# Kernel tuning notes

Hardware: AMD Instinct MI355X
Metric: run time of the kernel (lower is better)

## Reference

```python
import jax, jax.numpy as jnp
import numpy as np

N_NODES = 100000
N_EDGES = 800000
NUM_GRAPHS = 512
IN_DIM = 16
EDGE_DIM = 1
HID = 64       # emb_dim
MLP_H = 32     # hidden_layers inside each MPNNLayer
L = 3          # num_layers
EPS = 1e-5


def setup_inputs() -> dict:
    key = jax.random.key(0)
    ks = jax.random.split(key, 24)
    s = 0.05
    inp = {
        "x": jax.random.normal(ks[0], (N_NODES, IN_DIM), jnp.float32),
        "edge_index": jax.random.randint(ks[1], (2, N_EDGES), 0, N_NODES),
        "edge_attr": jax.random.uniform(ks[2], (N_EDGES, EDGE_DIM), jnp.float32),
        "batch": jnp.sort(jax.random.randint(ks[3], (N_NODES,), 0, NUM_GRAPHS)),
        # input projection
        "lin_in_w": jax.random.normal(ks[4], (IN_DIM, HID), jnp.float32) * s,
        "lin_in_b": jnp.zeros((HID,), jnp.float32),
        # message MLP (stacked over L layers): Linear(129->32), BN(32), ReLU, Linear(32->64), ReLU, BN(64)
        "msg_w1": jax.random.normal(ks[5], (L, 2 * HID + EDGE_DIM, MLP_H), jnp.float32) * s,
        "msg_b1": jnp.zeros((L, MLP_H), jnp.float32),
        "msg_g1": jnp.ones((L, MLP_H), jnp.float32),
        "msg_be1": jnp.zeros((L, MLP_H), jnp.float32),
        "msg_w2": jax.random.normal(ks[6], (L, MLP_H, HID), jnp.float32) * s,
        "msg_b2": jnp.zeros((L, HID), jnp.float32),
        "msg_g2": jnp.ones((L, HID), jnp.float32),
        "msg_be2": jnp.zeros((L, HID), jnp.float32),
        # update MLP: Linear(128->32), BN(32), ReLU, Linear(32->64), ReLU, BN(64)
        "upd_w1": jax.random.normal(ks[7], (L, 2 * HID, MLP_H), jnp.float32) * s,
        "upd_b1": jnp.zeros((L, MLP_H), jnp.float32),
        "upd_g1": jnp.ones((L, MLP_H), jnp.float32),
        "upd_be1": jnp.zeros((L, MLP_H), jnp.float32),
        "upd_w2": jax.random.normal(ks[8], (L, MLP_H, HID), jnp.float32) * s,
        "upd_b2": jnp.zeros((L, HID), jnp.float32),
        "upd_g2": jnp.ones((L, HID), jnp.float32),
        "upd_be2": jnp.zeros((L, HID), jnp.float32),
        # head Linear(64->1) + ReLU
        "out_w": jax.random.normal(ks[9], (HID, 1), jnp.float32) * s,
        "out_b": jnp.zeros((1,), jnp.float32),
    }
    return inp


def _bn(h, g, b):
    # BatchNorm1d, training-mode batch stats (biased variance), dropout treated as identity (eval)
    mu = jnp.mean(h, axis=0)
    var = jnp.var(h, axis=0)
    return g * (h - mu) * jax.lax.rsqrt(var + EPS) + b


def reference(x, edge_index, edge_attr, batch,
              lin_in_w, lin_in_b,
              msg_w1, msg_b1, msg_g1, msg_be1, msg_w2, msg_b2, msg_g2, msg_be2,
              upd_w1, upd_b1, upd_g1, upd_be1, upd_w2, upd_b2, upd_g2, upd_be2,
              out_w, out_b):
    src = edge_index[0]  # x_j source
    dst = edge_index[1]  # x_i target / aggregation index
    h = x @ lin_in_w + lin_in_b  # [N, HID]
    for l in range(L):
        # message: cat([x_i, x_j, edge_attr]) -> Linear -> BN -> ReLU -> Linear -> ReLU -> BN
        m_in = jnp.concatenate([h[dst], h[src], edge_attr], axis=1)  # [E, 2*HID+EDGE_DIM]
        m = jax.nn.relu(_bn(m_in @ msg_w1[l] + msg_b1[l], msg_g1[l], msg_be1[l]))
        m = _bn(jax.nn.relu(m @ msg_w2[l] + msg_b2[l]), msg_g2[l], msg_be2[l])
        # aggregate: scatter-add over destination nodes
        agg = jax.ops.segment_sum(m, dst, num_segments=N_NODES)  # [N, HID]
        # update: cat([x, aggr]) -> Linear -> BN -> ReLU -> Linear -> ReLU -> BN
        u_in = jnp.concatenate([h, agg], axis=1)  # [N, 2*HID]
        u = jax.nn.relu(_bn(u_in @ upd_w1[l] + upd_b1[l], upd_g1[l], upd_be1[l]))
        u = _bn(jax.nn.relu(u @ upd_w2[l] + upd_b2[l]), upd_g2[l], upd_be2[l])
        h = h + u  # residual (x += conv(...))
    # global mean pool
    pooled = jax.ops.segment_sum(h, batch, num_segments=NUM_GRAPHS)
    counts = jax.ops.segment_sum(jnp.ones((h.shape[0],), h.dtype), batch, num_segments=NUM_GRAPHS)
    pooled = pooled / jnp.maximum(counts, 1.0)[:, None]
    return jax.nn.relu(pooled @ out_w + out_b).reshape(-1)  # [NUM_GRAPHS]
```

## Files before the change

### kernel.cpp

```cpp
#include <hip/hip_runtime.h>
#include <hip/hip_bf16.h>

#define N_NODES   100000
#define N_EDGES   800000
#define NUM_GRAPHS 512
#define IN_DIM    16
#define HID       64
#define MLP_H     32
#define EPS       1e-5f
#define TPB       256
#define SCAN_B    1024
#define NCHUNK    ((N_NODES + SCAN_B - 1) / SCAN_B)
#define GSB       2048
#define NWAVES    (GSB * 4)
#define PER_W     ((N_EDGES + NWAVES - 1) / NWAVES)
#define NODEBLKS  ((N_NODES + 63) / 64)

using nh2   = decltype(__builtin_amdgcn_cvt_pkrtz(0.f, 0.f));
typedef _Float16 f16x8 __attribute__((ext_vector_type(8)));
typedef float    f32x4 __attribute__((ext_vector_type(4)));
typedef int      i32x4 __attribute__((ext_vector_type(4)));

__device__ __forceinline__ nh2 pack2(float a, float b) {
  return __builtin_amdgcn_cvt_pkrtz(a, b);
}
__device__ __forceinline__ float wsum(float v) {
  v += __shfl_xor(v, 1, 64);
  v += __shfl_xor(v, 2, 64);
  v += __shfl_xor(v, 4, 64);
  v += __shfl_xor(v, 8, 64);
  v += __shfl_xor(v, 16, 64);
  v += __shfl_xor(v, 32, 64);
  return v;
}
__device__ __forceinline__ int lbound(const int* __restrict__ rs, int key) {
  int lo = 0, hi = N_NODES;
  while (lo < hi) { int m = (lo + hi) >> 1; if (rs[m] < key) lo = m + 1; else hi = m; }
  return lo;
}

__global__ __launch_bounds__(TPB) void k_deg(const int* __restrict__ ei, int* __restrict__ deg) {
  int e = blockIdx.x * TPB + threadIdx.x;
  if (e < N_EDGES) atomicAdd(&deg[ei[N_EDGES + e]], 1);
}

__global__ __launch_bounds__(SCAN_B) void k_scan_part(const int* __restrict__ deg,
                                                      int* __restrict__ partials) {
  __shared__ int red[SCAN_B];
  int i = blockIdx.x * SCAN_B + threadIdx.x;
  red[threadIdx.x] = (i < N_NODES) ? deg[i] : 0;
  __syncthreads();
  for (int off = SCAN_B / 2; off > 0; off >>= 1) {
    if (threadIdx.x < off) red[threadIdx.x] += red[threadIdx.x + off];
    __syncthreads();
  }
  if (threadIdx.x == 0) partials[blockIdx.x] = red[0];
}

__global__ void k_scan_mid(int* __restrict__ partials, int* __restrict__ row_start) {
  int run = 0;
  for (int b = 0; b < NCHUNK; ++b) { int t = partials[b]; partials[b] = run; run += t; }
  row_start[N_NODES] = run;
}

__global__ __launch_bounds__(SCAN_B) void k_scan_fin(const int* __restrict__ deg,
                                                     const int* __restrict__ partials,
                                                     int* __restrict__ row_start,
                                                     int* __restrict__ cursor) {
  __shared__ int buf[2][SCAN_B];
  int t = threadIdx.x, i = blockIdx.x * SCAN_B + t;
  int v = (i < N_NODES) ? deg[i] : 0;
  buf[0][t] = v;
  __syncthreads();
  int cur = 0;
  for (int off = 1; off < SCAN_B; off <<= 1) {
    int nv = buf[cur][t] + ((t >= off) ? buf[cur][t - off] : 0);
    buf[cur ^ 1][t] = nv; cur ^= 1;
    __syncthreads();
  }
  if (i < N_NODES) {
    int excl = buf[cur][t] - v + partials[blockIdx.x];
    row_start[i] = excl;
    cursor[i] = excl;
  }
}

__global__ __launch_bounds__(TPB) void k_fill(const int* __restrict__ ei,
                                              const float* __restrict__ ea,
                                              int* __restrict__ cursor,
                                              i32x4* __restrict__ erec) {
  int e = blockIdx.x * TPB + threadIdx.x;
  if (e >= N_EDGES) return;
  int dst = ei[N_EDGES + e];
  int pos = atomicAdd(&cursor[dst], 1);
  i32x4 rec;
  rec[0] = ei[e];
  rec[1] = dst;
  rec[2] = __float_as_int(ea[e]);
  rec[3] = 0;
  erec[pos] = rec;
}

__global__ __launch_bounds__(TPB) void k_lin_in(const float* __restrict__ x,
                                                const float* __restrict__ w,
                                                const float* __restrict__ b,
                                                float* __restrict__ h) {
  int i = blockIdx.x * TPB + threadIdx.x;
  if (i >= N_NODES) return;
  float xi[IN_DIM];
  const float4* xp = reinterpret_cast<const float4*>(x + i * IN_DIM);
#pragma unroll
  for (int q = 0; q < 4; ++q) {
    float4 v = xp[q];
    xi[4*q] = v.x; xi[4*q+1] = v.y; xi[4*q+2] = v.z; xi[4*q+3] = v.w;
  }
  float4* hp = reinterpret_cast<float4*>(h + i * HID);
#pragma unroll
  for (int j4 = 0; j4 < HID/4; ++j4) {
    float o[4];
#pragma unroll
    for (int c = 0; c < 4; ++c) {
      int j = j4*4 + c;
      float acc = b[j];
#pragma unroll
      for (int k = 0; k < IN_DIM; ++k) acc += xi[k] * w[k*HID + j];
      o[c] = acc;
    }
    float4 ov = {o[0], o[1], o[2], o[3]};
    hp[j4] = ov;
  }
}

__global__ __launch_bounds__(TPB) void k_pq(const float* __restrict__ h,
                                            const float* __restrict__ w1,
                                            const float* __restrict__ b1,
                                            float* __restrict__ P,
                                            _Float16* __restrict__ Qh) {
  const int part = __builtin_amdgcn_readfirstlane(threadIdx.x >> 6);
  const int lane = threadIdx.x & 63;
  const int i = blockIdx.x * 64 + lane;
  if (i >= N_NODES) return;
  const int jb = (part & 1) * 16;
  const bool isQ = part >= 2;
  const float* wbase = w1 + (isQ ? 64 * MLP_H : 0) + jb;
  float acc[16];
#pragma unroll
  for (int j = 0; j < 16; ++j) acc[j] = isQ ? 0.f : b1[jb + j];
  const float4* hp = reinterpret_cast<const float4*>(h + i * HID);
#pragma unroll 4
  for (int k4 = 0; k4 < 16; ++k4) {
    float4 a = hp[k4];
    const float* wr = wbase + (k4*4) * MLP_H;
#pragma unroll
    for (int j = 0; j < 16; ++j)
      acc[j] += a.x*wr[j] + a.y*wr[MLP_H+j] + a.z*wr[2*MLP_H+j] + a.w*wr[3*MLP_H+j];
  }
  if (!isQ) {
    float4* pp = reinterpret_cast<float4*>(P + i * MLP_H + jb);
#pragma unroll
    for (int c = 0; c < 4; ++c) {
      float4 o = {acc[4*c], acc[4*c+1], acc[4*c+2], acc[4*c+3]};
      pp[c] = o;
    }
  } else {
    i32x4 o0, o1;
#pragma unroll
    for (int c = 0; c < 4; ++c) {
      o0[c] = __builtin_bit_cast(int, pack2(acc[2*c],     acc[2*c+1]));
      o1[c] = __builtin_bit_cast(int, pack2(acc[8+2*c],   acc[8+2*c+1]));
    }
    i32x4* qp = reinterpret_cast<i32x4*>(Qh + i * MLP_H + jb);
    qp[0] = o0; qp[1] = o1;
  }
}

__global__ __launch_bounds__(TPB) void k_gather(const float* __restrict__ P,
                                                const _Float16* __restrict__ Qh,
                                                const i32x4* __restrict__ erec,
                                                const float* __restrict__ w1,
                                                _Float16* __restrict__ z1h,
                                                float* __restrict__ gstat) {
  const int lane = threadIdx.x & 63;
  const int kq  = lane & 15;
  const int qtr = lane >> 4;
  const float wk0 = w1[128 * MLP_H + 2*kq];
  const float wk1 = w1[128 * MLP_H + 2*kq + 1];
  const int* Qi = (const int*)Qh;
  int* z1i = (int*)z1h;
  float s0 = 0.f, s1 = 0.f, qa0 = 0.f, qa1 = 0.f;
  const int wv = blockIdx.x * 4 + (threadIdx.x >> 6);
  const int c0 = wv * PER_W;
  const int c1 = min(c0 + PER_W, N_EDGES);
  if (c0 < N_EDGES) {
    const int c1m1 = c1 - 1;
    const int rounds = (c1 - c0 + 3) >> 2;
#define EIDX(R) min(c0 + 4*(R) + qtr, c1m1)
    i32x4 rec2 = erec[EIDX(0)];
    i32x4 rec3 = erec[EIDX(1)];
    i32x4 recH = erec[EIDX(2)];
    int   qiA = Qi[rec2[0] * 16 + kq];
    float2 pA = *reinterpret_cast<const float2*>(P + rec2[1] * MLP_H + 2*kq);
    float  aA = __int_as_float(rec2[2]);
    int   qiB = Qi[rec3[0] * 16 + kq];
    float2 pB = *reinterpret_cast<const float2*>(P + rec3[1] * MLP_H + 2*kq);
    float  aB = __int_as_float(rec3[2]);
    for (int r = 0; r < rounds; ++r) {
      i32x4 recN = erec[EIDX(r + 3)];
      int   qiC = Qi[recH[0] * 16 + kq];
      float2 pC = *reinterpret_cast<const float2*>(P + recH[1] * MLP_H + 2*kq);
      float  aC = __int_as_float(recH[2]);
      const int e = c0 + 4*r + qtr;
      nh2 hv = __builtin_bit_cast(nh2, qiA);
      float z0 = pA.x + (float)hv.x + aA * wk0;
      float z1 = pA.y + (float)hv.y + aA * wk1;
      if (e < c1) {
        z1i[min(e, c1m1) * 16 + kq] = __builtin_bit_cast(int, pack2(z0, z1));
        s0 += z0; s1 += z1;
        qa0 = fmaf(z0, z0, qa0); qa1 = fmaf(z1, z1, qa1);
      }
      qiA = qiB; pA = pB; aA = aB;
      qiB = qiC; pB = pC; aB = aC;
      recH = recN;
    }
#undef EIDX
  }
  s0  += __shfl_xor(s0, 16, 64);  s0  += __shfl_xor(s0, 32, 64);
  s1  += __shfl_xor(s1, 16, 64);  s1  += __shfl_xor(s1, 32, 64);
  qa0 += __shfl_xor(qa0, 16, 64); qa0 += __shfl_xor(qa0, 32, 64);
  qa1 += __shfl_xor(qa1, 16, 64); qa1 += __shfl_xor(qa1, 32, 64);
  __shared__ float ls[4][MLP_H], lq[4][MLP_H];
  const int w = threadIdx.x >> 6;
  if (lane < 16) {
    ls[w][2*lane] = s0; ls[w][2*lane+1] = s1;
    lq[w][2*lane] = qa0; lq[w][2*lane+1] = qa1;
  }
  __syncthreads();
  const int t = threadIdx.x;
  if (t < MLP_H)
    unsafeAtomicAdd(&gstat[t], ls[0][t] + ls[1][t] + ls[2][t] + ls[3][t]);
  else if (t < 2*MLP_H)
    unsafeAtomicAdd(&gstat[t], lq[0][t-MLP_H] + lq[1][t-MLP_H] + lq[2][t-MLP_H] + lq[3][t-MLP_H]);
}

__global__ __launch_bounds__(TPB) void k_msgdot(const _Float16* __restrict__ z1h,
                                                const int* __restrict__ rs,
                                                const float* __restrict__ gstat_in,
                                                const float* __restrict__ g1,
                                                const float* __restrict__ be1,
                                                const float* __restrict__ w2,
                                                const float* __restrict__ b2,
                                                float* __restrict__ agg,
                                                float* __restrict__ gstat_out) {
  const int lane = threadIdx.x & 63;
  const int col = lane & 15;
  const int g   = lane >> 4;
  float a1v[8], c1v[8];
#pragma unroll
  for (int i = 0; i < 8; ++i) {
    int kf = g*8 + i;
    float mu = gstat_in[kf] * (1.f / N_EDGES);
    float var = fmaxf(gstat_in[MLP_H + kf] * (1.f / N_EDGES) - mu * mu, 0.f);
    float a = g1[kf] * rsqrtf(var + EPS);
    a1v[i] = a; c1v[i] = be1[kf] - a * mu;
  }
  f16x8 bf0, bf1, bf2, bf3;
#define MKB(BF, C) { i32x4 bw; \
  _Pragma("unroll") for (int ii = 0; ii < 4; ++ii) { \
    nh2 p = pack2(w2[(g*8 + 2*ii) * HID + (C)*16 + col], \
                  w2[(g*8 + 2*ii + 1) * HID + (C)*16 + col]); \
    bw[ii] = __builtin_bit_cast(int, p); } \
  BF = __builtin_bit_cast(f16x8, bw); }
  MKB(bf0, 0) MKB(bf1, 1) MKB(bf2, 2) MKB(bf3, 3)
#undef MKB
  float b2c[4];
#pragma unroll
  for (int c = 0; c < 4; ++c) b2c[c] = b2[c*16 + col];

  float sacc[4] = {0.f,0.f,0.f,0.f}, qacc[4] = {0.f,0.f,0.f,0.f};
  const int wv = blockIdx.x * 4 + (threadIdx.x >> 6);
  const int key0 = min(wv * PER_W, N_EDGES);
  const int key1 = min((wv + 1) * PER_W, N_EDGES);
  const int n0 = lbound(rs, key0);
  const int n1 = (wv == NWAVES - 1) ? N_NODES : lbound(rs, key1);

  for (int n = n0; n < n1; ++n) {
    const int start = rs[n], end = rs[n + 1];
    float aggacc[4] = {0.f,0.f,0.f,0.f};
    for (int t0 = start; t0 < end; t0 += 16) {
      const int ec = min(t0 + col, end - 1);
      f16x8 zv = *reinterpret_cast<const f16x8*>(z1h + ec * MLP_H + g * 8);
      i32x4 aw;
#pragma unroll
      for (int i = 0; i < 4; ++i) {
        float m0 = fmaxf(fmaf(a1v[2*i],   (float)zv[2*i],   c1v[2*i]),   0.f);
        float m1 = fmaxf(fmaf(a1v[2*i+1], (float)zv[2*i+1], c1v[2*i+1]), 0.f);
        aw[i] = __builtin_bit_cast(int, pack2(m0, m1));
      }
      f16x8 af = __builtin_bit_cast(f16x8, aw);
      f32x4 zc = {0.f,0.f,0.f,0.f};
      f32x4 cc0 = __builtin_amdgcn_mfma_f32_16x16x32_f16(af, bf0, zc, 0, 0, 0);
      f32x4 cc1 = __builtin_amdgcn_mfma_f32_16x16x32_f16(af, bf1, zc, 0, 0, 0);
      f32x4 cc2 = __builtin_amdgcn_mfma_f32_16x16x32_f16(af, bf2, zc, 0, 0, 0);
      f32x4 cc3 = __builtin_amdgcn_mfma_f32_16x16x32_f16(af, bf3, zc, 0, 0, 0);
      bool vld[4];
#pragma unroll
      for (int reg = 0; reg < 4; ++reg) vld[reg] = (t0 + g*4 + reg) < end;
#define EPI(CC, CI) { \
  _Pragma("unroll") for (int reg = 0; reg < 4; ++reg) { \
    float tv = fmaxf(CC[reg] + b2c[CI], 0.f); \
    tv = vld[reg] ? tv : 0.f; \
    aggacc[CI] += tv; qacc[CI] = fmaf(tv, tv, qacc[CI]); } }
      EPI(cc0, 0) EPI(cc1, 1) EPI(cc2, 2) EPI(cc3, 3)
#undef EPI
    }
#pragma unroll
    for (int c = 0; c < 4; ++c) sacc[c] += aggacc[c];
#pragma unroll
    for (int c = 0; c < 4; ++c) {
      aggacc[c] += __shfl_xor(aggacc[c], 16, 64);
      aggacc[c] += __shfl_xor(aggacc[c], 32, 64);
    }
    float aout = (g == 0) ? aggacc[0] : (g == 1) ? aggacc[1] : (g == 2) ? aggacc[2] : aggacc[3];
    agg[n * HID + g * 16 + col] = aout;
  }
#pragma unroll
  for (int c = 0; c < 4; ++c) {
    sacc[c] += __shfl_xor(sacc[c], 16, 64);
    sacc[c] += __shfl_xor(sacc[c], 32, 64);
    qacc[c] += __shfl_xor(qacc[c], 16, 64);
    qacc[c] += __shfl_xor(qacc[c], 32, 64);
  }
  __shared__ float ls[4][HID], lq[4][HID];
  const int w = threadIdx.x >> 6;
  if (g == 0) {
#pragma unroll
    for (int c = 0; c < 4; ++c) { ls[w][c*16 + col] = sacc[c]; lq[w][c*16 + col] = qacc[c]; }
  }
  __syncthreads();
  const int t = threadIdx.x;
  if (t < HID)
    unsafeAtomicAdd(&gstat_out[t], ls[0][t] + ls[1][t] + ls[2][t] + ls[3][t]);
  else if (t < 2*HID)
    unsafeAtomicAdd(&gstat_out[t], lq[0][t-HID] + lq[1][t-HID] + lq[2][t-HID] + lq[3][t-HID]);
}

__global__ __launch_bounds__(TPB) void k_upd1(const float* __restrict__ h,
                                              const float* __restrict__ agg,
                                              const int* __restrict__ deg,
                                              const float* __restrict__ gstat_in,
                                              const float* __restrict__ g2,
                                              const float* __restrict__ be2,
                                              const float* __restrict__ w1,
                                              const float* __restrict__ b1,
                                              float* __restrict__ zu1) {
  __shared__ float sa[HID], sc[HID];
  {
    int t = threadIdx.x;
    if (t < HID) {
      float mu = gstat_in[t] * (1.f / N_EDGES);
      float var = fmaxf(gstat_in[HID + t] * (1.f / N_EDGES) - mu * mu, 0.f);
      float a = g2[t] * rsqrtf(var + EPS);
      sa[t] = a; sc[t] = be2[t] - a * mu;
    }
  }
  __syncthreads();
  const int widx = __builtin_amdgcn_readfirstlane(threadIdx.x >> 6);
  const int part = widx & 1;
  const int grp  = blockIdx.x * 2 + (widx >> 1);
  const int lane = threadIdx.x & 63;
  const int jb = part * 16;
  const int i = grp * 64 + lane;
  if (i >= N_NODES) return;
  float acc[16];
#pragma unroll
  for (int j = 0; j < 16; ++j) acc[j] = b1[jb + j];
  const float4* hp = reinterpret_cast<const float4*>(h + i * HID);
#pragma unroll 4
  for (int k4 = 0; k4 < 16; ++k4) {
    float4 a = hp[k4];
    const float* wr = w1 + (k4*4) * MLP_H + jb;
#pragma unroll
    for (int j = 0; j < 16; ++j)
      acc[j] += a.x*wr[j] + a.y*wr[MLP_H+j] + a.z*wr[2*MLP_H+j] + a.w*wr[3*MLP_H+j];
  }
  float degf = (float)deg[i];
  const float4* ap = reinterpret_cast<const float4*>(agg + i * HID);
#pragma unroll 4
  for (int k4 = 0; k4 < 16; ++k4) {
    float4 g4 = ap[k4];
    int k = k4*4;
    float a0 = sa[k]  *g4.x + sc[k]  *degf;
    float a1 = sa[k+1]*g4.y + sc[k+1]*degf;
    float a2 = sa[k+2]*g4.z + sc[k+2]*degf;
    float a3 = sa[k+3]*g4.w + sc[k+3]*degf;
    const float* wr = w1 + (64 + k) * MLP_H + jb;
#pragma unroll
    for (int j = 0; j < 16; ++j)
      acc[j] += a0*wr[j] + a1*wr[MLP_H+j] + a2*wr[2*MLP_H+j] + a3*wr[3*MLP_H+j];
  }
  float4* zp = reinterpret_cast<float4*>(zu1 + i * MLP_H + jb);
#pragma unroll
  for (int c = 0; c < 4; ++c) {
    float4 o = {acc[4*c], acc[4*c+1], acc[4*c+2], acc[4*c+3]};
    zp[c] = o;
  }
}

__global__ __launch_bounds__(TPB) void k_upd2(const float* __restrict__ zu1,
                                              const float* __restrict__ gstat_in,
                                              const float* __restrict__ gu1,
                                              const float* __restrict__ beu1,
                                              const float* __restrict__ w2,
                                              const float* __restrict__ b2,
                                              float* __restrict__ tu) {
  __shared__ float sa[MLP_H], sc[MLP_H];
  {
    int t = threadIdx.x;
    if (t < MLP_H) {
      float mu = gstat_in[t] * (1.f / N_NODES);
      float var = fmaxf(gstat_in[MLP_H + t] * (1.f / N_NODES) - mu * mu, 0.f);
      float a = gu1[t] * rsqrtf(var + EPS);
      sa[t] = a; sc[t] = beu1[t] - a * mu;
    }
  }
  __syncthreads();
  const int widx = __builtin_amdgcn_readfirstlane(threadIdx.x >> 6);
  const int part = widx & 1;
  const int grp  = blockIdx.x * 2 + (widx >> 1);
  const int lane = threadIdx.x & 63;
  const int jb = part * 32;
  const int i = grp * 64 + lane;
  if (i >= N_NODES) return;
  float m1[MLP_H];
  const float4* zp = reinterpret_cast<const float4*>(zu1 + i * MLP_H);
#pragma unroll
  for (int c = 0; c < MLP_H/4; ++c) {
    float4 z = zp[c];
    int kk = 4*c;
    m1[kk]   = fmaxf(sa[kk]  *z.x + sc[kk],   0.f);
    m1[kk+1] = fmaxf(sa[kk+1]*z.y + sc[kk+1], 0.f);
    m1[kk+2] = fmaxf(sa[kk+2]*z.z + sc[kk+2], 0.f);
    m1[kk+3] = fmaxf(sa[kk+3]*z.w + sc[kk+3], 0.f);
  }
#pragma unroll
  for (int j4 = 0; j4 < 8; ++j4) {
    float tv[4];
#pragma unroll
    for (int c = 0; c < 4; ++c) {
      int j = jb + j4*4 + c;
      float v = b2[j];
#pragma unroll
      for (int kk = 0; kk < MLP_H; ++kk) v += m1[kk] * w2[kk*HID + j];
      tv[c] = fmaxf(v, 0.f);
    }
    float4 o = {tv[0], tv[1], tv[2], tv[3]};
    *reinterpret_cast<float4*>(tu + i * HID + jb + j4*4) = o;
  }
}

template <int NF>
__global__ __launch_bounds__(TPB) void k_colstats(const float* __restrict__ X,
                                                  int nrows, float* __restrict__ gstat) {
  const int RPB = TPB / NF;
  int f = threadIdx.x % NF;
  int rloc = threadIdx.x / NF;
  float s = 0.f, q = 0.f;
  for (int r = blockIdx.x * RPB + rloc; r < nrows; r += gridDim.x * RPB) {
    float v = X[r * NF + f];
    s += v; q = fmaf(v, v, q);
  }
  __shared__ float ls[TPB], lq[TPB];
  ls[threadIdx.x] = s; lq[threadIdx.x] = q;
  __syncthreads();
  if (threadIdx.x < NF) {
    float ss = 0.f, qq = 0.f;
#pragma unroll
    for (int r = 0; r < RPB; ++r) { ss += ls[r*NF + f]; qq += lq[r*NF + f]; }
    unsafeAtomicAdd(&gstat[f], ss);
    unsafeAtomicAdd(&gstat[NF + f], qq);
  }
}

__global__ __launch_bounds__(TPB) void k_resid(float* __restrict__ h,
                                               const float* __restrict__ tu,
                                               const float* __restrict__ gstat_in,
                                               const float* __restrict__ gu2,
                                               const float* __restrict__ beu2) {
  __shared__ float sa[HID], sc[HID];
  {
    int t = threadIdx.x;
    if (t < HID) {
      float mu = gstat_in[t] * (1.f / N_NODES);
      float var = fmaxf(gstat_in[HID + t] * (1.f / N_NODES) - mu * mu, 0.f);
      float a = gu2[t] * rsqrtf(var + EPS);
      sa[t] = a; sc[t] = beu2[t] - a * mu;
    }
  }
  __syncthreads();
  int idx = blockIdx.x * TPB + threadIdx.x;
  if (idx >= N_NODES * (HID/4)) return;
  int j0 = (idx & (HID/4 - 1)) * 4;
  float4 hv = reinterpret_cast<const float4*>(h)[idx];
  float4 tv = reinterpret_cast<const float4*>(tu)[idx];
  hv.x += sa[j0]  *tv.x + sc[j0];
  hv.y += sa[j0+1]*tv.y + sc[j0+1];
  hv.z += sa[j0+2]*tv.z + sc[j0+2];
  hv.w += sa[j0+3]*tv.w + sc[j0+3];
  reinterpret_cast<float4*>(h)[idx] = hv;
}

__global__ __launch_bounds__(TPB) void k_pool_head(const float* __restrict__ h,
                                                   const int* __restrict__ batch,
                                                   const float* __restrict__ ow,
                                                   const float* __restrict__ ob,
                                                   float* __restrict__ out) {
  int g = blockIdx.x;
  int lo = 0, hi = N_NODES;
  while (lo < hi) { int mid = (lo+hi) >> 1; if (batch[mid] < g) lo = mid+1; else hi = mid; }
  int start = lo;
  lo = start; hi = N_NODES;
  while (lo < hi) { int mid = (lo+hi) >> 1; if (batch[mid] < g+1) lo = mid+1; else hi = mid; }
  int end = lo;
  int j = threadIdx.x & 63;
  int sub = threadIdx.x >> 6;
  float acc = 0.f;
  for (int n = start + sub; n < end; n += 4) acc += h[n*HID + j];
  __shared__ float red[TPB];
  red[threadIdx.x] = acc;
  __syncthreads();
  if (threadIdx.x < 64) {
    float s = red[threadIdx.x] + red[64+threadIdx.x] + red[128+threadIdx.x] + red[192+threadIdx.x];
    float cnt = (float)(end - start);
    float pooled = s / fmaxf(cnt, 1.0f);
    float v = pooled * ow[threadIdx.x];
    v = wsum(v);
    if (threadIdx.x == 0) out[g] = fmaxf(v + ob[0], 0.f);
  }
}

extern "C" void kernel_launch(void* const* d_in, const int* in_sizes, int n_in,
                              void* d_out, int out_size, void* d_ws, size_t ws_size,
                              hipStream_t stream) {
  const float* x       = (const float*)d_in[0];
  const int*   ei      = (const int*)  d_in[1];
  const float* ea      = (const float*)d_in[2];
  const int*   batch   = (const int*)  d_in[3];
  const float* lin_w   = (const float*)d_in[4];
  const float* lin_b   = (const float*)d_in[5];
  const float* msg_w1  = (const float*)d_in[6];
  const float* msg_b1  = (const float*)d_in[7];
  const float* msg_g1  = (const float*)d_in[8];
  const float* msg_be1 = (const float*)d_in[9];
  const float* msg_w2  = (const float*)d_in[10];
  const float* msg_b2  = (const float*)d_in[11];
  const float* msg_g2  = (const float*)d_in[12];
  const float* msg_be2 = (const float*)d_in[13];
  const float* upd_w1  = (const float*)d_in[14];
  const float* upd_b1  = (const float*)d_in[15];
  const float* upd_g1  = (const float*)d_in[16];
  const float* upd_be1 = (const float*)d_in[17];
  const float* upd_w2  = (const float*)d_in[18];
  const float* upd_b2  = (const float*)d_in[19];
  const float* upd_g2  = (const float*)d_in[20];
  const float* upd_be2 = (const float*)d_in[21];
  const float* out_w   = (const float*)d_in[22];
  const float* out_b   = (const float*)d_in[23];
  float* out = (float*)d_out;

  float* W     = (float*)d_ws;
  float* h     = W;
  float* P     = W + 6400000;
  _Float16* Qh = (_Float16*)(W + 9600000);
  float* agg   = W + 12800000;
  _Float16* z1h = (_Float16*)(W + 19200000);
  float* zu1   = W + 32000000;
  float* tu    = W + 35200000;
  float* stats = W + 41600000;
  int*   ib    = (int*)(W + 41601152);
  int* deg       = ib;
  int* row_start = ib + 100000;
  int* cursor    = ib + 200001;
  int* partials  = ib + 300001;
  i32x4* erec    = (i32x4*)(ib + 300232);

  hipMemsetAsync(stats, 0, 3*384*sizeof(float), stream);
  hipMemsetAsync(deg, 0, N_NODES*sizeof(int), stream);

  k_deg<<<N_EDGES/TPB, TPB, 0, stream>>>(ei, deg);
  k_scan_part<<<NCHUNK, SCAN_B, 0, stream>>>(deg, partials);
  k_scan_mid<<<1, 1, 0, stream>>>(partials, row_start);
  k_scan_fin<<<NCHUNK, SCAN_B, 0, stream>>>(deg, partials, row_start, cursor);
  k_fill<<<N_EDGES/TPB, TPB, 0, stream>>>(ei, ea, cursor, erec);

  k_lin_in<<<(N_NODES+TPB-1)/TPB, TPB, 0, stream>>>(x, lin_w, lin_b, h);

  const int PQ_BLKS   = NODEBLKS;
  const int UPD_BLKS  = (NODEBLKS + 1) / 2;

  for (int l = 0; l < 3; ++l) {
    const float* mw1 = msg_w1 + (size_t)l*129*MLP_H;
    const float* mb1 = msg_b1 + l*MLP_H;
    const float* mg1 = msg_g1 + l*MLP_H;
    const float* mbe1= msg_be1 + l*MLP_H;
    const float* mw2 = msg_w2 + (size_t)l*MLP_H*HID;
    const float* mb2 = msg_b2 + l*HID;
    const float* mg2 = msg_g2 + l*HID;
    const float* mbe2= msg_be2 + l*HID;
    const float* uw1 = upd_w1 + (size_t)l*128*MLP_H;
    const float* ub1 = upd_b1 + l*MLP_H;
    const float* ug1 = upd_g1 + l*MLP_H;
    const float* ube1= upd_be1 + l*MLP_H;
    const float* uw2 = upd_w2 + (size_t)l*MLP_H*HID;
    const float* ub2 = upd_b2 + l*HID;
    const float* ug2 = upd_g2 + l*HID;
    const float* ube2= upd_be2 + l*HID;
    float* st = stats + l*384;

    k_pq<<<PQ_BLKS, TPB, 0, stream>>>(h, mw1, mb1, P, Qh);
    k_gather<<<GSB, TPB, 0, stream>>>(P, Qh, erec, mw1, z1h, st);
    k_msgdot<<<GSB, TPB, 0, stream>>>(z1h, row_start, st, mg1, mbe1, mw2, mb2, agg, st+64);
    k_upd1<<<UPD_BLKS, TPB, 0, stream>>>(h, agg, deg, st+64, mg2, mbe2, uw1, ub1, zu1);
    k_colstats<MLP_H><<<512, TPB, 0, stream>>>(zu1, N_NODES, st+192);
    k_upd2<<<UPD_BLKS, TPB, 0, stream>>>(zu1, st+192, ug1, ube1, uw2, ub2, tu);
    k_colstats<HID><<<512, TPB, 0, stream>>>(tu, N_NODES, st+256);
    k_resid<<<(N_NODES*(HID/4)+TPB-1)/TPB, TPB, 0, stream>>>(h, tu, st+256, ug2, ube2);
  }

  k_pool_head<<<NUM_GRAPHS, TPB, 0, stream>>>(h, batch, out_w, out_b, out);
}
```

Measured before the change: 964.2 us.

## Recompute first message layer in msgdot instead of storing fp16 z1 intermediate

The gather kernel now only accumulates BN statistics of the first message-layer preactivation and no longer writes the per-edge fp16 z1 buffer. The msgdot kernel recomputes z1 on the fly from P (per destination node, hoisted), gathered Qh rows and edge attributes, with BN folded into the affine terms. Both kernels use 16-byte vector loads. This removes an 800k×32 fp16 write and reread per layer but gathers Qh twice, adding random-access traffic and extra ALU work in msgdot.

```diff
diff --git a/kernel.cpp b/kernel.cpp
--- a/kernel.cpp
+++ b/kernel.cpp
@@ -178,61 +178,68 @@
                                                 const _Float16* __restrict__ Qh,
                                                 const i32x4* __restrict__ erec,
                                                 const float* __restrict__ w1,
-                                                _Float16* __restrict__ z1h,
                                                 float* __restrict__ gstat) {
   const int lane = threadIdx.x & 63;
-  const int kq  = lane & 15;
-  const int qtr = lane >> 4;
-  const float wk0 = w1[128 * MLP_H + 2*kq];
-  const float wk1 = w1[128 * MLP_H + 2*kq + 1];
-  const int* Qi = (const int*)Qh;
-  int* z1i = (int*)z1h;
-  float s0 = 0.f, s1 = 0.f, qa0 = 0.f, qa1 = 0.f;
+  const int fg   = lane & 3;
+  const int sl   = lane >> 2;
+  const int fb   = fg * 8;
+  float wk[8];
+#pragma unroll
+  for (int i = 0; i < 8; ++i) wk[i] = w1[128 * MLP_H + fb + i];
+  float sv[8], qs[8];
+#pragma unroll
+  for (int i = 0; i < 8; ++i) { sv[i] = 0.f; qs[i] = 0.f; }
   const int wv = blockIdx.x * 4 + (threadIdx.x >> 6);
   const int c0 = wv * PER_W;
   const int c1 = min(c0 + PER_W, N_EDGES);
   if (c0 < N_EDGES) {
     const int c1m1 = c1 - 1;
-    const int rounds = (c1 - c0 + 3) >> 2;
-#define EIDX(R) min(c0 + 4*(R) + qtr, c1m1)
-    i32x4 rec2 = erec[EIDX(0)];
-    i32x4 rec3 = erec[EIDX(1)];
+    const int rounds = (c1 - c0 + 15) >> 4;
+#define EIDX(R) min(c0 + 16*(R) + sl, c1m1)
+    i32x4 recA = erec[EIDX(0)];
+    i32x4 recB = erec[EIDX(1)];
     i32x4 recH = erec[EIDX(2)];
-    int   qiA = Qi[rec2[0] * 16 + kq];
-    float2 pA = *reinterpret_cast<const float2*>(P + rec2[1] * MLP_H + 2*kq);
-    float  aA = __int_as_float(rec2[2]);
-    int   qiB = Qi[rec3[0] * 16 + kq];
-    float2 pB = *reinterpret_cast<const float2*>(P + rec3[1] * MLP_H + 2*kq);
-    float  aB = __int_as_float(rec3[2]);
+    f16x8 qA  = *reinterpret_cast<const f16x8*>(Qh + recA[0] * MLP_H + fb);
+    f32x4 pA0 = *reinterpret_cast<const f32x4*>(P + recA[1] * MLP_H + fb);
+    f32x4 pA1 = *reinterpret_cast<const f32x4*>(P + recA[1] * MLP_H + fb + 4);
+    float aA  = __int_as_float(recA[2]);
+    f16x8 qB  = *reinterpret_cast<const f16x8*>(Qh + recB[0] * MLP_H + fb);
+    f32x4 pB0 = *reinterpret_cast<const f32x4*>(P + recB[1] * MLP_H + fb);
+    f32x4 pB1 = *reinterpret_cast<const f32x4*>(P + recB[1] * MLP_H + fb + 4);
+    float aB  = __int_as_float(recB[2]);
     for (int r = 0; r < rounds; ++r) {
       i32x4 recN = erec[EIDX(r + 3)];
-      int   qiC = Qi[recH[0] * 16 + kq];
-      float2 pC = *reinterpret_cast<const float2*>(P + recH[1] * MLP_H + 2*kq);
-      float  aC = __int_as_float(recH[2]);
-      const int e = c0 + 4*r + qtr;
-      nh2 hv = __builtin_bit_cast(nh2, qiA);
-      float z0 = pA.x + (float)hv.x + aA * wk0;
-      float z1 = pA.y + (float)hv.y + aA * wk1;
-      if (e < c1) {
-        z1i[min(e, c1m1) * 16 + kq] = __builtin_bit_cast(int, pack2(z0, z1));
-        s0 += z0; s1 += z1;
-        qa0 = fmaf(z0, z0, qa0); qa1 = fmaf(z1, z1, qa1);
+      f16x8 qC  = *reinterpret_cast<const f16x8*>(Qh + recH[0] * MLP_H + fb);
+      f32x4 pC0 = *reinterpret_cast<const f32x4*>(P + recH[1] * MLP_H + fb);
+      f32x4 pC1 = *reinterpret_cast<const f32x4*>(P + recH[1] * MLP_H + fb + 4);
+      float aC  = __int_as_float(recH[2]);
+      const bool vc = (c0 + 16*r + sl) < c1;
+      if (vc) {
+#pragma unroll
+        for (int i = 0; i < 8; ++i) {
+          float pv = (i < 4) ? pA0[i] : pA1[i - 4];
+          float z = fmaf(aA, wk[i], pv) + (float)qA[i];
+          sv[i] += z; qs[i] = fmaf(z, z, qs[i]);
+        }
       }
-      qiA = qiB; pA = pB; aA = aB;
-      qiB = qiC; pB = pC; aB = aC;
+      qA = qB; pA0 = pB0; pA1 = pB1; aA = aB;
+      qB = qC; pB0 = pC0; pB1 = pC1; aB = aC;
       recH = recN;
     }
 #undef EIDX
   }
-  s0  += __shfl_xor(s0, 16, 64);  s0  += __shfl_xor(s0, 32, 64);
-  s1  += __shfl_xor(s1, 16, 64);  s1  += __shfl_xor(s1, 32, 64);
-  qa0 += __shfl_xor(qa0, 16, 64); qa0 += __shfl_xor(qa0, 32, 64);
-  qa1 += __shfl_xor(qa1, 16, 64); qa1 += __shfl_xor(qa1, 32, 64);
+#pragma unroll
+  for (int i = 0; i < 8; ++i) {
+    sv[i] += __shfl_xor(sv[i], 4, 64);  sv[i] += __shfl_xor(sv[i], 8, 64);
+    sv[i] += __shfl_xor(sv[i], 16, 64); sv[i] += __shfl_xor(sv[i], 32, 64);
+    qs[i] += __shfl_xor(qs[i], 4, 64);  qs[i] += __shfl_xor(qs[i], 8, 64);
+    qs[i] += __shfl_xor(qs[i], 16, 64); qs[i] += __shfl_xor(qs[i], 32, 64);
+  }
   __shared__ float ls[4][MLP_H], lq[4][MLP_H];
   const int w = threadIdx.x >> 6;
-  if (lane < 16) {
-    ls[w][2*lane] = s0; ls[w][2*lane+1] = s1;
-    lq[w][2*lane] = qa0; lq[w][2*lane+1] = qa1;
+  if (lane < 4) {
+#pragma unroll
+    for (int i = 0; i < 8; ++i) { ls[w][fb + i] = sv[i]; lq[w][fb + i] = qs[i]; }
   }
   __syncthreads();
   const int t = threadIdx.x;
@@ -242,11 +249,14 @@
     unsafeAtomicAdd(&gstat[t], lq[0][t-MLP_H] + lq[1][t-MLP_H] + lq[2][t-MLP_H] + lq[3][t-MLP_H]);
 }
 
-__global__ __launch_bounds__(TPB) void k_msgdot(const _Float16* __restrict__ z1h,
+__global__ __launch_bounds__(TPB) void k_msgdot(const i32x4* __restrict__ erec,
+                                                const _Float16* __restrict__ Qh,
+                                                const float* __restrict__ P,
                                                 const int* __restrict__ rs,
                                                 const float* __restrict__ gstat_in,
                                                 const float* __restrict__ g1,
                                                 const float* __restrict__ be1,
+                                                const float* __restrict__ w1,
                                                 const float* __restrict__ w2,
                                                 const float* __restrict__ b2,
                                                 float* __restrict__ agg,
@@ -254,7 +264,7 @@
   const int lane = threadIdx.x & 63;
   const int col = lane & 15;
   const int g   = lane >> 4;
-  float a1v[8], c1v[8];
+  float a1v[8], c1v[8], aw[8];
 #pragma unroll
   for (int i = 0; i < 8; ++i) {
     int kf = g*8 + i;
@@ -262,6 +272,7 @@
     float var = fmaxf(gstat_in[MLP_H + kf] * (1.f / N_EDGES) - mu * mu, 0.f);
     float a = g1[kf] * rsqrtf(var + EPS);
     a1v[i] = a; c1v[i] = be1[kf] - a * mu;
+    aw[i] = a * w1[128 * MLP_H + kf];
   }
   f16x8 bf0, bf1, bf2, bf3;
 #define MKB(BF, C) { i32x4 bw; \
@@ -283,45 +294,59 @@
   const int n0 = lbound(rs, key0);
   const int n1 = (wv == NWAVES - 1) ? N_NODES : lbound(rs, key1);
 
-  for (int n = n0; n < n1; ++n) {
-    const int start = rs[n], end = rs[n + 1];
-    float aggacc[4] = {0.f,0.f,0.f,0.f};
-    for (int t0 = start; t0 < end; t0 += 16) {
-      const int ec = min(t0 + col, end - 1);
-      f16x8 zv = *reinterpret_cast<const f16x8*>(z1h + ec * MLP_H + g * 8);
-      i32x4 aw;
-#pragma unroll
-      for (int i = 0; i < 4; ++i) {
-        float m0 = fmaxf(fmaf(a1v[2*i],   (float)zv[2*i],   c1v[2*i]),   0.f);
-        float m1 = fmaxf(fmaf(a1v[2*i+1], (float)zv[2*i+1], c1v[2*i+1]), 0.f);
-        aw[i] = __builtin_bit_cast(int, pack2(m0, m1));
-      }
-      f16x8 af = __builtin_bit_cast(f16x8, aw);
-      f32x4 zc = {0.f,0.f,0.f,0.f};
-      f32x4 cc0 = __builtin_amdgcn_mfma_f32_16x16x32_f16(af, bf0, zc, 0, 0, 0);
-      f32x4 cc1 = __builtin_amdgcn_mfma_f32_16x16x32_f16(af, bf1, zc, 0, 0, 0);
-      f32x4 cc2 = __builtin_amdgcn_mfma_f32_16x16x32_f16(af, bf2, zc, 0, 0, 0);
-      f32x4 cc3 = __builtin_amdgcn_mfma_f32_16x16x32_f16(af, bf3, zc, 0, 0, 0);
-      bool vld[4];
-#pragma unroll
-      for (int reg = 0; reg < 4; ++reg) vld[reg] = (t0 + g*4 + reg) < end;
+  if (n0 < n1) {
+    const int eLast = rs[n1] - 1;
+    i32x4 rec = erec[min(rs[n0] + col, eLast)];
+    f16x8 qv = *reinterpret_cast<const f16x8*>(Qh + rec[0] * MLP_H + g * 8);
+    for (int n = n0; n < n1; ++n) {
+      const int start = rs[n], end = rs[n + 1];
+      f32x4 p0 = *reinterpret_cast<const f32x4*>(P + n * MLP_H + g * 8);
+      f32x4 p1 = *reinterpret_cast<const f32x4*>(P + n * MLP_H + g * 8 + 4);
+      float pb[8];
+#pragma unroll
+      for (int i = 0; i < 8; ++i)
+        pb[i] = fmaf(a1v[i], (i < 4) ? p0[i] : p1[i - 4], c1v[i]);
+      float aggacc[4] = {0.f,0.f,0.f,0.f};
+      for (int t0 = start; t0 < end; t0 += 16) {
+        const int bnext = (t0 + 16 < end) ? (t0 + 16) : end;
+        i32x4 recN = erec[min(bnext + col, eLast)];
+        const float ea = __int_as_float(rec[2]);
+        i32x4 awb;
+#pragma unroll
+        for (int i = 0; i < 4; ++i) {
+          float m0 = fmaxf(fmaf(a1v[2*i],   (float)qv[2*i],   fmaf(ea, aw[2*i],   pb[2*i])),   0.f);
+          float m1 = fmaxf(fmaf(a1v[2*i+1], (float)qv[2*i+1], fmaf(ea, aw[2*i+1], pb[2*i+1])), 0.f);
+          awb[i] = __builtin_bit_cast(int, pack2(m0, m1));
+        }
+        f16x8 af = __builtin_bit_cast(f16x8, awb);
+        f32x4 zc = {0.f,0.f,0.f,0.f};
+        f32x4 cc0 = __builtin_amdgcn_mfma_f32_16x16x32_f16(af, bf0, zc, 0, 0, 0);
+        f32x4 cc1 = __builtin_amdgcn_mfma_f32_16x16x32_f16(af, bf1, zc, 0, 0, 0);
+        f32x4 cc2 = __builtin_amdgcn_mfma_f32_16x16x32_f16(af, bf2, zc, 0, 0, 0);
+        f32x4 cc3 = __builtin_amdgcn_mfma_f32_16x16x32_f16(af, bf3, zc, 0, 0, 0);
+        f16x8 qvN = *reinterpret_cast<const f16x8*>(Qh + recN[0] * MLP_H + g * 8);
+        bool vld[4];
+#pragma unroll
+        for (int reg = 0; reg < 4; ++reg) vld[reg] = (t0 + g*4 + reg) < end;
 #define EPI(CC, CI) { \
   _Pragma("unroll") for (int reg = 0; reg < 4; ++reg) { \
     float tv = fmaxf(CC[reg] + b2c[CI], 0.f); \
     tv = vld[reg] ? tv : 0.f; \
     aggacc[CI] += tv; qacc[CI] = fmaf(tv, tv, qacc[CI]); } }
-      EPI(cc0, 0) EPI(cc1, 1) EPI(cc2, 2) EPI(cc3, 3)
+        EPI(cc0, 0) EPI(cc1, 1) EPI(cc2, 2) EPI(cc3, 3)
 #undef EPI
-    }
-#pragma unroll
-    for (int c = 0; c < 4; ++c) sacc[c] += aggacc[c];
-#pragma unroll
-    for (int c = 0; c < 4; ++c) {
-      aggacc[c] += __shfl_xor(aggacc[c], 16, 64);
-      aggacc[c] += __shfl_xor(aggacc[c], 32, 64);
-    }
-    float aout = (g == 0) ? aggacc[0] : (g == 1) ? aggacc[1] : (g == 2) ? aggacc[2] : aggacc[3];
-    agg[n * HID + g * 16 + col] = aout;
+        rec = recN; qv = qvN;
+      }
+#pragma unroll
+      for (int c = 0; c < 4; ++c) sacc[c] += aggacc[c];
+#pragma unroll
+      for (int c = 0; c < 4; ++c) {
+        aggacc[c] += __shfl_xor(aggacc[c], 16, 64);
+        aggacc[c] += __shfl_xor(aggacc[c], 32, 64);
+      }
+      float aout = (g == 0) ? aggacc[0] : (g == 1) ? aggacc[1] : (g == 2) ? aggacc[2] : aggacc[3];
+      agg[n * HID + g * 16 + col] = aout;
+    }
   }
 #pragma unroll
   for (int c = 0; c < 4; ++c) {
@@ -572,7 +597,6 @@
   float* P     = W + 6400000;
   _Float16* Qh = (_Float16*)(W + 9600000);
   float* agg   = W + 12800000;
-  _Float16* z1h = (_Float16*)(W + 19200000);
   float* zu1   = W + 32000000;
   float* tu    = W + 35200000;
   float* stats = W + 41600000;
@@ -617,8 +641,9 @@
     float* st = stats + l*384;
 
     k_pq<<<PQ_BLKS, TPB, 0, stream>>>(h, mw1, mb1, P, Qh);
-    k_gather<<<GSB, TPB, 0, stream>>>(P, Qh, erec, mw1, z1h, st);
-    k_msgdot<<<GSB, TPB, 0, stream>>>(z1h, row_start, st, mg1, mbe1, mw2, mb2, agg, st+64);
+    k_gather<<<GSB, TPB, 0, stream>>>(P, Qh, erec, mw1, st);
+    k_msgdot<<<GSB, TPB, 0, stream>>>(erec, Qh, P, row_start, st, mg1, mbe1, mw1, mw2, mb2,
+                                      agg, st+64);
     k_upd1<<<UPD_BLKS, TPB, 0, stream>>>(h, agg, deg, st+64, mg2, mbe2, uw1, ub1, zu1);
     k_colstats<MLP_H><<<512, TPB, 0, stream>>>(zu1, N_NODES, st+192);
     k_upd2<<<UPD_BLKS, TPB, 0, stream>>>(zu1, st+192, ug1, ube1, uw2, ub2, tu);
```

Measured after the change: 1.005 ms. 1.04x slower.
